# Optimization experiments

Hardware: AMD Instinct MI355X
Metric: run time of the kernel (lower is better)

## Reference

```python
import jax, jax.numpy as jnp
import numpy as np

D_MODEL = 256
N_HEAD = 8
D_FF = 2048
BATCH = 4
TOK_PER_BATCH = 4096
N = BATCH * TOK_PER_BATCH  # 16384 total queries == total keys
L = 32  # neighbors per query
EPS = 1e-5


def _layer_norm(x, g, b):
    mu = jnp.mean(x, axis=-1, keepdims=True)
    var = jnp.mean(jnp.square(x - mu), axis=-1, keepdims=True)
    return (x - mu) * jax.lax.rsqrt(var + EPS) * g + b


def setup_inputs() -> dict:
    key = jax.random.key(0)
    ks = jax.random.split(key, 16)
    d, f = D_MODEL, D_FF
    s = 1.0 / np.sqrt(d)
    inp = {
        "src": jax.random.normal(ks[0], (N, d), dtype=jnp.float32),
        "index_pair": jax.random.randint(ks[1], (N, L), 0, TOK_PER_BATCH, dtype=jnp.int64),
        "query_batch_cnt": jnp.full((BATCH,), TOK_PER_BATCH, dtype=jnp.int32),
        "key_batch_cnt": jnp.full((BATCH,), TOK_PER_BATCH, dtype=jnp.int32),
        "index_pair_batch": jnp.repeat(jnp.arange(BATCH, dtype=jnp.int32), TOK_PER_BATCH),
        "Wq": jax.random.normal(ks[2], (d, d), dtype=jnp.float32) * s,
        "bq": jnp.zeros((d,), jnp.float32),
        "Wk": jax.random.normal(ks[3], (d, d), dtype=jnp.float32) * s,
        "bk": jnp.zeros((d,), jnp.float32),
        "Wv": jax.random.normal(ks[4], (d, d), dtype=jnp.float32) * s,
        "bv": jnp.zeros((d,), jnp.float32),
        "Wo": jax.random.normal(ks[5], (d, d), dtype=jnp.float32) * s,
        "bo": jnp.zeros((d,), jnp.float32),
        "W1": jax.random.normal(ks[6], (d, f), dtype=jnp.float32) * s,
        "b1": jnp.zeros((f,), jnp.float32),
        "W2": jax.random.normal(ks[7], (f, d), dtype=jnp.float32) * (1.0 / np.sqrt(f)),
        "b2": jnp.zeros((d,), jnp.float32),
        "g1": jnp.ones((d,), jnp.float32),
        "be1": jnp.zeros((d,), jnp.float32),
        "g2": jnp.ones((d,), jnp.float32),
        "be2": jnp.zeros((d,), jnp.float32),
    }
    return inp


def _attention(src, index_pair, key_batch_cnt, index_pair_batch,
               Wq, bq, Wk, bk, Wv, bv, Wo, bo):
    n, d = src.shape
    hd = d // N_HEAD
    scale = hd ** -0.5
    q = (src @ Wq + bq).reshape(n, N_HEAD, hd) * scale
    k = src @ Wk + bk
    v = src @ Wv + bv
    # exclusive cumsum -> start offset of each batch's key segment
    key_start = jnp.cumsum(key_batch_cnt) - key_batch_cnt          # [B]
    offs = key_start[index_pair_batch]                             # [N]
    valid = index_pair >= 0                                        # [N, L]
    idx = jnp.where(valid, index_pair + offs[:, None].astype(index_pair.dtype), 0)
    kg = k[idx].reshape(n, L, N_HEAD, hd)                          # gathered keys
    vg = v[idx].reshape(n, L, N_HEAD, hd)                          # gathered values
    logits = jnp.einsum("nhd,nlhd->nhl", q, kg)
    logits = jnp.where(valid[:, None, :], logits, jnp.float32(-1e9))
    attn = jax.nn.softmax(logits, axis=-1)
    out = jnp.einsum("nhl,nlhd->nhd", attn, vg).reshape(n, d)
    return out @ Wo + bo


def reference(src, index_pair, query_batch_cnt, key_batch_cnt, index_pair_batch,
              Wq, bq, Wk, bk, Wv, bv, Wo, bo, W1, b1, W2, b2, g1, be1, g2, be2):
    src2 = _attention(src, index_pair, key_batch_cnt, index_pair_batch,
                      Wq, bq, Wk, bk, Wv, bv, Wo, bo)
    x = _layer_norm(src + src2, g1, be1)
    ff = jax.nn.relu(x @ W1 + b1) @ W2 + b2
    return _layer_norm(x + ff, g2, be2)
```

## Files before the change

### kernel.cpp

```cpp
#include <hip/hip_runtime.h>
#include <hip/hip_bf16.h>
#include <cstddef>
#include <cstdint>

#define D_MODEL 256
#define N_TOK   16384
#define NHEAD   8
#define HDIM    32
#define LNEIGH  32
#define DFF     2048

typedef short bf16x8 __attribute__((ext_vector_type(8)));
typedef float f32x4  __attribute__((ext_vector_type(4)));

__device__ __forceinline__ float b2f(short s) {
    unsigned u = ((unsigned)(unsigned short)s) << 16;
    return __builtin_bit_cast(float, u);
}

__device__ __forceinline__ void gload_lds16(const void* g, void* l) {
    auto* gp = reinterpret_cast<const __attribute__((address_space(1))) uint32_t*>(
        reinterpret_cast<uintptr_t>(g));
    auto* lp = reinterpret_cast<__attribute__((address_space(3))) uint32_t*>(
        reinterpret_cast<uintptr_t>(l));
    __builtin_amdgcn_global_load_lds(gp, lp, 16, 0, 0);
}

__global__ __launch_bounds__(256) void gemm_bt(
    const __hip_bfloat16* __restrict__ A, int lda,
    const __hip_bfloat16* __restrict__ Bt, int ldb,
    const float* __restrict__ bias,
    __hip_bfloat16* __restrict__ outb,
    int M, int N, int K, int relu)
{
    __shared__ short Asm[2][128 * 32];
    __shared__ short Bsm[2][128 * 32];

    const int tid  = threadIdx.x;
    const int lane = tid & 63;
    const int wid  = tid >> 6;
    const int wr   = wid >> 1;
    const int wc   = wid & 1;
    const int bm   = blockIdx.y * 128;
    const int bn   = blockIdx.x * 128;

    f32x4 acc[4][4] = {};
    const int srow = lane >> 2;
    const int seg  = (lane & 3) * 8;

    auto stage = [&](int buf, int k0) {
        #pragma unroll
        for (int t = 0; t < 2; ++t) {
            int rbase = wid * 32 + t * 16;
            gload_lds16(A  + (size_t)(bm + rbase + srow) * lda + k0 + seg, &Asm[buf][rbase * 32]);
            gload_lds16(Bt + (size_t)(bn + rbase + srow) * ldb + k0 + seg, &Bsm[buf][rbase * 32]);
        }
    };

    const int nk = K >> 5;
    stage(0, 0);
    __syncthreads();

    for (int kk = 0; kk < nk; ++kk) {
        const int cur = kk & 1;
        if (kk + 1 < nk) stage(cur ^ 1, (kk + 1) << 5);

        bf16x8 a[4], b[4];
        #pragma unroll
        for (int i = 0; i < 4; ++i)
            a[i] = *(const bf16x8*)&Asm[cur][(wr * 64 + i * 16 + (lane & 15)) * 32 + (lane >> 4) * 8];
        #pragma unroll
        for (int j = 0; j < 4; ++j)
            b[j] = *(const bf16x8*)&Bsm[cur][(wc * 64 + j * 16 + (lane & 15)) * 32 + (lane >> 4) * 8];
        #pragma unroll
        for (int i = 0; i < 4; ++i)
            #pragma unroll
            for (int j = 0; j < 4; ++j)
                acc[i][j] = __builtin_amdgcn_mfma_f32_16x16x32_bf16(a[i], b[j], acc[i][j], 0, 0, 0);
        __syncthreads();
    }

    #pragma unroll
    for (int i = 0; i < 4; ++i) {
        int rbase = bm + wr * 64 + i * 16 + ((lane >> 4) << 2);
        #pragma unroll
        for (int j = 0; j < 4; ++j) {
            int col = bn + wc * 64 + j * 16 + (lane & 15);
            float bval = bias ? bias[col] : 0.0f;
            #pragma unroll
            for (int r = 0; r < 4; ++r) {
                int row = rbase + r;
                float v = acc[i][j][r] + bval;
                if (relu) v = fmaxf(v, 0.0f);
                outb[(size_t)row * N + col] = __float2bfloat16(v);
            }
        }
    }
}

__global__ __launch_bounds__(256) void gemm_qkv(
    const __hip_bfloat16* __restrict__ A,
    const __hip_bfloat16* __restrict__ Bt,
    const float* __restrict__ bias,
    float* __restrict__ qf,
    __hip_bfloat16* __restrict__ kvb)
{
    __shared__ short Asm[2][128 * 32];
    __shared__ short Bsm[2][128 * 32];

    const int tid  = threadIdx.x;
    const int lane = tid & 63;
    const int wid  = tid >> 6;
    const int wr   = wid >> 1;
    const int wc   = wid & 1;
    const int bm   = blockIdx.y * 128;
    const int bn   = blockIdx.x * 128;

    f32x4 acc[4][4] = {};
    const int srow = lane >> 2;
    const int seg  = (lane & 3) * 8;

    auto stage = [&](int buf, int k0) {
        #pragma unroll
        for (int t = 0; t < 2; ++t) {
            int rbase = wid * 32 + t * 16;
            gload_lds16(A  + (size_t)(bm + rbase + srow) * 256 + k0 + seg, &Asm[buf][rbase * 32]);
            gload_lds16(Bt + (size_t)(bn + rbase + srow) * 256 + k0 + seg, &Bsm[buf][rbase * 32]);
        }
    };

    stage(0, 0);
    __syncthreads();
    for (int kk = 0; kk < 8; ++kk) {
        const int cur = kk & 1;
        if (kk + 1 < 8) stage(cur ^ 1, (kk + 1) << 5);
        bf16x8 a[4], b[4];
        #pragma unroll
        for (int i = 0; i < 4; ++i)
            a[i] = *(const bf16x8*)&Asm[cur][(wr * 64 + i * 16 + (lane & 15)) * 32 + (lane >> 4) * 8];
        #pragma unroll
        for (int j = 0; j < 4; ++j)
            b[j] = *(const bf16x8*)&Bsm[cur][(wc * 64 + j * 16 + (lane & 15)) * 32 + (lane >> 4) * 8];
        #pragma unroll
        for (int i = 0; i < 4; ++i)
            #pragma unroll
            for (int j = 0; j < 4; ++j)
                acc[i][j] = __builtin_amdgcn_mfma_f32_16x16x32_bf16(a[i], b[j], acc[i][j], 0, 0, 0);
        __syncthreads();
    }

    const bool isq = (bn < 256);
    #pragma unroll
    for (int i = 0; i < 4; ++i) {
        int rbase = bm + wr * 64 + i * 16 + ((lane >> 4) << 2);
        #pragma unroll
        for (int j = 0; j < 4; ++j) {
            int col = bn + wc * 64 + j * 16 + (lane & 15);
            float bval = bias[col];
            #pragma unroll
            for (int r = 0; r < 4; ++r) {
                int row = rbase + r;
                float v = acc[i][j][r] + bval;
                if (isq) qf[(size_t)row * 256 + col] = v;
                else     kvb[(size_t)row * 512 + (col - 256)] = __float2bfloat16(v);
            }
        }
    }
}

__global__ __launch_bounds__(512) void gemm_bt_ln8(
    const __hip_bfloat16* __restrict__ A, int lda,
    const __hip_bfloat16* __restrict__ Bt, int ldb,
    const float* __restrict__ bias,
    const float* __restrict__ residf,
    const __hip_bfloat16* __restrict__ residb,
    const float* __restrict__ g,
    const float* __restrict__ be,
    float* __restrict__ outf,
    __hip_bfloat16* __restrict__ outb,
    int K)
{
    __shared__ short Asm[2][64 * 32];
    __shared__ short Bsm[2][256 * 32];
    __shared__ float lnS[8][64], lnS2[8][64];
    __shared__ float rmu[64], rrs[64];

    const int tid  = threadIdx.x;
    const int lane = tid & 63;
    const int wid  = tid >> 6;
    const int wr   = wid >> 2;
    const int wc   = wid & 3;
    const int bm   = blockIdx.x * 64;
    const int lo   = lane & 15;
    const int hi   = lane >> 4;

    f32x4 acc[2][4] = {};
    const int srow = lane >> 2;
    const int seg  = (lane & 3) * 8;

    auto stage = [&](int buf, int k0) {
        if (wid < 4) {
            int ra = wid * 16;
            gload_lds16(A + (size_t)(bm + ra + srow) * lda + k0 + seg, &Asm[buf][ra * 32]);
        }
        #pragma unroll
        for (int t = 0; t < 2; ++t) {
            int rb = wid * 32 + t * 16;
            gload_lds16(Bt + (size_t)(rb + srow) * ldb + k0 + seg, &Bsm[buf][rb * 32]);
        }
    };

    const int nk = K >> 5;
    stage(0, 0);
    __syncthreads();

    for (int kk = 0; kk < nk; ++kk) {
        const int cur = kk & 1;
        if (kk + 1 < nk) stage(cur ^ 1, (kk + 1) << 5);

        bf16x8 a[2], b[4];
        #pragma unroll
        for (int i = 0; i < 2; ++i)
            a[i] = *(const bf16x8*)&Asm[cur][(wr * 32 + i * 16 + lo) * 32 + hi * 8];
        #pragma unroll
        for (int j = 0; j < 4; ++j)
            b[j] = *(const bf16x8*)&Bsm[cur][(wc * 64 + j * 16 + lo) * 32 + hi * 8];
        #pragma unroll
        for (int i = 0; i < 2; ++i)
            #pragma unroll
            for (int j = 0; j < 4; ++j)
                acc[i][j] = __builtin_amdgcn_mfma_f32_16x16x32_bf16(a[i], b[j], acc[i][j], 0, 0, 0);
        __syncthreads();
    }

    float ps[2][4] = {}, ps2[2][4] = {};
    #pragma unroll
    for (int j = 0; j < 4; ++j) {
        int col = wc * 64 + j * 16 + lo;
        float bval = bias ? bias[col] : 0.0f;
        #pragma unroll
        for (int i = 0; i < 2; ++i) {
            #pragma unroll
            for (int r = 0; r < 4; ++r) {
                int row = bm + wr * 32 + i * 16 + hi * 4 + r;
                float v = acc[i][j][r] + bval;
                size_t o = (size_t)row * 256 + col;
                if (residf) v += residf[o];
                if (residb) v += __bfloat162float(residb[o]);
                acc[i][j][r] = v;
                ps[i][r]  += v;
                ps2[i][r] += v * v;
            }
        }
    }
    #pragma unroll
    for (int i = 0; i < 2; ++i)
        #pragma unroll
        for (int r = 0; r < 4; ++r) {
            #pragma unroll
            for (int m = 1; m < 16; m <<= 1) {
                ps[i][r]  += __shfl_xor(ps[i][r],  m);
                ps2[i][r] += __shfl_xor(ps2[i][r], m);
            }
        }
    if (lo == 0) {
        #pragma unroll
        for (int i = 0; i < 2; ++i)
            #pragma unroll
            for (int r = 0; r < 4; ++r) {
                int rl = wr * 32 + i * 16 + hi * 4 + r;
                lnS[wid][rl]  = ps[i][r];
                lnS2[wid][rl] = ps2[i][r];
            }
    }
    __syncthreads();
    if (tid < 64) {
        int base = (tid >> 5) * 4;
        float s  = lnS[base][tid] + lnS[base + 1][tid] + lnS[base + 2][tid] + lnS[base + 3][tid];
        float s2 = lnS2[base][tid] + lnS2[base + 1][tid] + lnS2[base + 2][tid] + lnS2[base + 3][tid];
        float mu  = s * (1.0f / 256.0f);
        float var = s2 * (1.0f / 256.0f) - mu * mu;
        rmu[tid] = mu;
        rrs[tid] = rsqrtf(var + 1e-5f);
    }
    __syncthreads();

    #pragma unroll
    for (int j = 0; j < 4; ++j) {
        int col = wc * 64 + j * 16 + lo;
        float gg = g[col], bb = be[col];
        #pragma unroll
        for (int i = 0; i < 2; ++i) {
            #pragma unroll
            for (int r = 0; r < 4; ++r) {
                int rl = wr * 32 + i * 16 + hi * 4 + r;
                float v = (acc[i][j][r] - rmu[rl]) * rrs[rl] * gg + bb;
                size_t o = (size_t)(bm + rl) * 256 + col;
                if (outf) outf[o] = v;
                if (outb) outb[o] = __float2bfloat16(v);
            }
        }
    }
}

__global__ __launch_bounds__(256) void cvt_f2b(
    const float* __restrict__ x, __hip_bfloat16* __restrict__ y, int n)
{
    int i = (blockIdx.x * 256 + threadIdx.x) * 4;
    if (i >= n) return;
    float4 v = *(const float4*)(x + i);
    y[i + 0] = __float2bfloat16(v.x);
    y[i + 1] = __float2bfloat16(v.y);
    y[i + 2] = __float2bfloat16(v.z);
    y[i + 3] = __float2bfloat16(v.w);
}

__global__ __launch_bounds__(256) void cvt_wt_tiled(
    const float* __restrict__ W, __hip_bfloat16* __restrict__ Wt,
    int K, int N, float scale)
{
    __shared__ float t[32][33];
    const int n0 = blockIdx.x * 32;
    const int k0 = blockIdx.y * 32;
    const int tx = threadIdx.x & 31;
    const int ty = threadIdx.x >> 5;
    #pragma unroll
    for (int i = 0; i < 32; i += 8)
        t[ty + i][tx] = W[(size_t)(k0 + ty + i) * N + n0 + tx];
    __syncthreads();
    #pragma unroll
    for (int i = 0; i < 32; i += 8)
        Wt[(size_t)(n0 + ty + i) * K + k0 + tx] = __float2bfloat16(t[tx][ty + i] * scale);
}

__global__ __launch_bounds__(256) void cvt_w3_tiled(
    const float* __restrict__ Wa, const float* __restrict__ Wb,
    const float* __restrict__ Wc, __hip_bfloat16* __restrict__ Wt,
    float scale_a)
{
    __shared__ float t[32][33];
    const int n0 = blockIdx.x * 32;
    const int k0 = blockIdx.y * 32;
    const float* W = (n0 < 256) ? Wa : (n0 < 512 ? Wb : Wc);
    const float sc = (n0 < 256) ? scale_a : 1.0f;
    const int ncol = n0 & 255;
    const int tx = threadIdx.x & 31;
    const int ty = threadIdx.x >> 5;
    #pragma unroll
    for (int i = 0; i < 32; i += 8)
        t[ty + i][tx] = W[(size_t)(k0 + ty + i) * 256 + ncol + tx];
    __syncthreads();
    #pragma unroll
    for (int i = 0; i < 32; i += 8)
        Wt[(size_t)(n0 + ty + i) * 256 + k0 + tx] = __float2bfloat16(t[tx][ty + i] * sc);
}

__global__ __launch_bounds__(768) void make_bqkv(
    const float* __restrict__ bq, const float* __restrict__ bk,
    const float* __restrict__ bv, const int* __restrict__ kbc, int nb,
    float* __restrict__ o, int* __restrict__ ks, float qs)
{
    int i = threadIdx.x;
    if (i < 256)      o[i] = bq[i] * qs;
    else if (i < 512) o[i] = bk[i - 256];
    else              o[i] = bv[i - 512];
    if (i < nb) {
        int acc = 0;
        for (int j = 0; j < i; ++j) acc += kbc[j];
        ks[i] = acc;
    }
}

__global__ __launch_bounds__(256) void attn_wave(
    const float* __restrict__ qf,
    const __hip_bfloat16* __restrict__ kvb,
    const int* __restrict__ index_pair,
    const int* __restrict__ ipb,
    const int* __restrict__ key_start,
    __hip_bfloat16* __restrict__ out)
{
    const int w    = threadIdx.x >> 6;
    const int lane = threadIdx.x & 63;
    const int bid  = blockIdx.x;
    const int n  = (bid & 7) * 2048 + (bid >> 3) * 4 + w;
    const int c  = lane & 31;
    const int pp = lane >> 5;

    int raw = index_pair[(size_t)n * LNEIGH + c];
    int ks  = key_start[ipb[n]];
    int gi0 = (raw >= 0) ? raw + ks : -1;

    const float* qp = qf + (size_t)n * 256 + c * 8;
    float4 q0 = *(const float4*)(qp);
    float4 q1 = *(const float4*)(qp + 4);

    int gi[16];
    #pragma unroll
    for (int i = 0; i < 16; ++i) gi[i] = __shfl(gi0, 2 * i + pp);

    bf16x8 kr[16];
    #pragma unroll
    for (int i = 0; i < 16; ++i) {
        int g = gi[i] < 0 ? 0 : gi[i];
        kr[i] = *(const bf16x8*)(kvb + (size_t)g * 512 + c * 8);
    }

    float s[16];
    #pragma unroll
    for (int i = 0; i < 16; ++i) {
        float t = q0.x * b2f(kr[i][0]) + q0.y * b2f(kr[i][1])
                + q0.z * b2f(kr[i][2]) + q0.w * b2f(kr[i][3])
                + q1.x * b2f(kr[i][4]) + q1.y * b2f(kr[i][5])
                + q1.z * b2f(kr[i][6]) + q1.w * b2f(kr[i][7]);
        t += __shfl_xor(t, 1);
        t += __shfl_xor(t, 2);
        s[i] = (gi[i] < 0) ? -1e9f : t;
    }

    bf16x8 vr[16];
    #pragma unroll
    for (int i = 0; i < 16; ++i) {
        int g = gi[i] < 0 ? 0 : gi[i];
        vr[i] = *(const bf16x8*)(kvb + (size_t)g * 512 + 256 + c * 8);
    }

    float m = s[0];
    #pragma unroll
    for (int i = 1; i < 16; ++i) m = fmaxf(m, s[i]);
    m = fmaxf(m, __shfl_xor(m, 32));
    float tot = 0.0f;
    #pragma unroll
    for (int i = 0; i < 16; ++i) { s[i] = __expf(s[i] - m); tot += s[i]; }
    tot += __shfl_xor(tot, 32);
    const float inv = 1.0f / tot;

    float a[8] = {};
    #pragma unroll
    for (int i = 0; i < 16; ++i) {
        float wt = s[i] * inv;
        #pragma unroll
        for (int j = 0; j < 8; ++j) a[j] += wt * b2f(vr[i][j]);
    }
    #pragma unroll
    for (int j = 0; j < 8; ++j) a[j] += __shfl_xor(a[j], 32);

    if (pp == 0) {
        bf16x8 ov;
        #pragma unroll
        for (int j = 0; j < 8; ++j)
            ov[j] = __builtin_bit_cast(short, __float2bfloat16(a[j]));
        *(bf16x8*)((short*)out + (size_t)n * 256 + c * 8) = ov;
    }
}

extern "C" void kernel_launch(void* const* d_in, const int* in_sizes, int n_in,
                              void* d_out, int out_size, void* d_ws, size_t ws_size,
                              hipStream_t stream)
{
    const float* src = (const float*)d_in[0];
    const int*   index_pair = (const int*)d_in[1];
    const int*   kbc = (const int*)d_in[3];
    const int*   ipb = (const int*)d_in[4];
    const float* Wq = (const float*)d_in[5];
    const float* bq = (const float*)d_in[6];
    const float* Wk = (const float*)d_in[7];
    const float* bk = (const float*)d_in[8];
    const float* Wv = (const float*)d_in[9];
    const float* bv = (const float*)d_in[10];
    const float* Wo = (const float*)d_in[11];
    const float* bo = (const float*)d_in[12];
    const float* W1 = (const float*)d_in[13];
    const float* b1 = (const float*)d_in[14];
    const float* W2 = (const float*)d_in[15];
    const float* b2 = (const float*)d_in[16];
    const float* g1 = (const float*)d_in[17];
    const float* be1 = (const float*)d_in[18];
    const float* g2 = (const float*)d_in[19];
    const float* be2 = (const float*)d_in[20];
    float* out = (float*)d_out;
    const int nb = in_sizes[3];

    char* ws = (char*)d_ws;
    const size_t O_SRCBF = 0;
    const size_t O_QF    = 8388608;
    const size_t O_KVB   = 25165824;
    const size_t O_ATTN  = 41943040;
    const size_t O_HC    = 0;
    const size_t O_XBF   = 67108864;
    const size_t O_WQKV  = 75497472;
    const size_t O_WO    = O_WQKV + 768 * 256 * 2;
    const size_t O_W1    = O_WO + 256 * 256 * 2;
    const size_t O_W2    = O_W1 + (size_t)DFF * 256 * 2;
    const size_t O_BQKV  = O_W2 + (size_t)DFF * 256 * 2;
    const size_t O_KS    = O_BQKV + 768 * 4;

    __hip_bfloat16* src_bf  = (__hip_bfloat16*)(ws + O_SRCBF);
    float*          qf      = (float*)(ws + O_QF);
    __hip_bfloat16* kvb     = (__hip_bfloat16*)(ws + O_KVB);
    __hip_bfloat16* attn_bf = (__hip_bfloat16*)(ws + O_ATTN);
    __hip_bfloat16* hc      = (__hip_bfloat16*)(ws + O_HC);
    __hip_bfloat16* x_bf    = (__hip_bfloat16*)(ws + O_XBF);
    __hip_bfloat16* WqkvT   = (__hip_bfloat16*)(ws + O_WQKV);
    __hip_bfloat16* WoT     = (__hip_bfloat16*)(ws + O_WO);
    __hip_bfloat16* W1T     = (__hip_bfloat16*)(ws + O_W1);
    __hip_bfloat16* W2T     = (__hip_bfloat16*)(ws + O_W2);
    float*          bqkv    = (float*)(ws + O_BQKV);
    int*            ksbuf   = (int*)(ws + O_KS);

    const dim3 blk(256);
    const float qscale = 0.17677669529663687f;

    cvt_f2b<<<N_TOK * D_MODEL / 4 / 256, blk, 0, stream>>>(src, src_bf, N_TOK * D_MODEL);
    cvt_w3_tiled<<<dim3(24, 8), blk, 0, stream>>>(Wq, Wk, Wv, WqkvT, qscale);
    cvt_wt_tiled<<<dim3(8, 8),  blk, 0, stream>>>(Wo, WoT, 256, 256, 1.0f);
    cvt_wt_tiled<<<dim3(64, 8), blk, 0, stream>>>(W1, W1T, 256, DFF, 1.0f);
    cvt_wt_tiled<<<dim3(8, 64), blk, 0, stream>>>(W2, W2T, DFF, 256, 1.0f);
    make_bqkv<<<1, 768, 0, stream>>>(bq, bk, bv, kbc, nb, bqkv, ksbuf, qscale);

    gemm_qkv<<<dim3(6, 128), blk, 0, stream>>>(src_bf, WqkvT, bqkv, qf, kvb);

    attn_wave<<<dim3(N_TOK / 4), blk, 0, stream>>>(qf, kvb, index_pair, ipb, ksbuf, attn_bf);

    gemm_bt_ln8<<<dim3(N_TOK / 64), dim3(512), 0, stream>>>(
        attn_bf, 256, WoT, 256, bo, src, nullptr, g1, be1,
        nullptr, x_bf, 256);

    gemm_bt<<<dim3(16, 128), blk, 0, stream>>>(
        x_bf, 256, W1T, 256, b1, hc, N_TOK, DFF, 256, 1);

    gemm_bt_ln8<<<dim3(N_TOK / 64), dim3(512), 0, stream>>>(
        hc, DFF, W2T, DFF, b2, nullptr, x_bf, g2, be2,
        out, nullptr, DFF);
}
```

Before: 169.4 us.

## Load GEMM+LayerNorm operands straight from global memory and pad hidden leading dimension

The fused GEMM+LayerNorm kernel no longer stages A and B tiles through shared memory. Each wave now loads its MFMA fragments directly from global memory, which removes the LDS traffic and the per-step barriers. The FFN hidden activation and transposed W2 get a padded leading dimension (2080 instead of 2048) to break power-of-two strides that would otherwise cause channel or cache conflicts on the direct loads. The cost is that B fragments are reread from global/L2 by every wave with no shared reuse, and the loads are strided gathers rather than coalesced tiles.

Measured after the change: 202.8 us. +19.7%, slower.

```diff
diff --git a/kernel.cpp b/kernel.cpp
--- a/kernel.cpp
+++ b/kernel.cpp
@@ -9,6 +9,7 @@
 #define HDIM    32
 #define LNEIGH  32
 #define DFF     2048
+#define HCP     2080
 
 typedef short bf16x8 __attribute__((ext_vector_type(8)));
 typedef float f32x4  __attribute__((ext_vector_type(4)));
@@ -30,7 +31,7 @@
     const __hip_bfloat16* __restrict__ A, int lda,
     const __hip_bfloat16* __restrict__ Bt, int ldb,
     const float* __restrict__ bias,
-    __hip_bfloat16* __restrict__ outb,
+    __hip_bfloat16* __restrict__ outb, int ldc,
     int M, int N, int K, int relu)
 {
     __shared__ short Asm[2][128 * 32];
@@ -92,83 +93,13 @@
                 int row = rbase + r;
                 float v = acc[i][j][r] + bval;
                 if (relu) v = fmaxf(v, 0.0f);
-                outb[(size_t)row * N + col] = __float2bfloat16(v);
+                outb[(size_t)row * ldc + col] = __float2bfloat16(v);
             }
         }
     }
 }
 
-__global__ __launch_bounds__(256) void gemm_qkv(
-    const __hip_bfloat16* __restrict__ A,
-    const __hip_bfloat16* __restrict__ Bt,
-    const float* __restrict__ bias,
-    float* __restrict__ qf,
-    __hip_bfloat16* __restrict__ kvb)
-{
-    __shared__ short Asm[2][128 * 32];
-    __shared__ short Bsm[2][128 * 32];
-
-    const int tid  = threadIdx.x;
-    const int lane = tid & 63;
-    const int wid  = tid >> 6;
-    const int wr   = wid >> 1;
-    const int wc   = wid & 1;
-    const int bm   = blockIdx.y * 128;
-    const int bn   = blockIdx.x * 128;
-
-    f32x4 acc[4][4] = {};
-    const int srow = lane >> 2;
-    const int seg  = (lane & 3) * 8;
-
-    auto stage = [&](int buf, int k0) {
-        #pragma unroll
-        for (int t = 0; t < 2; ++t) {
-            int rbase = wid * 32 + t * 16;
-            gload_lds16(A  + (size_t)(bm + rbase + srow) * 256 + k0 + seg, &Asm[buf][rbase * 32]);
-            gload_lds16(Bt + (size_t)(bn + rbase + srow) * 256 + k0 + seg, &Bsm[buf][rbase * 32]);
-        }
-    };
-
-    stage(0, 0);
-    __syncthreads();
-    for (int kk = 0; kk < 8; ++kk) {
-        const int cur = kk & 1;
-        if (kk + 1 < 8) stage(cur ^ 1, (kk + 1) << 5);
-        bf16x8 a[4], b[4];
-        #pragma unroll
-        for (int i = 0; i < 4; ++i)
-            a[i] = *(const bf16x8*)&Asm[cur][(wr * 64 + i * 16 + (lane & 15)) * 32 + (lane >> 4) * 8];
-        #pragma unroll
-        for (int j = 0; j < 4; ++j)
-            b[j] = *(const bf16x8*)&Bsm[cur][(wc * 64 + j * 16 + (lane & 15)) * 32 + (lane >> 4) * 8];
-        #pragma unroll
-        for (int i = 0; i < 4; ++i)
-            #pragma unroll
-            for (int j = 0; j < 4; ++j)
-                acc[i][j] = __builtin_amdgcn_mfma_f32_16x16x32_bf16(a[i], b[j], acc[i][j], 0, 0, 0);
-        __syncthreads();
-    }
-
-    const bool isq = (bn < 256);
-    #pragma unroll
-    for (int i = 0; i < 4; ++i) {
-        int rbase = bm + wr * 64 + i * 16 + ((lane >> 4) << 2);
-        #pragma unroll
-        for (int j = 0; j < 4; ++j) {
-            int col = bn + wc * 64 + j * 16 + (lane & 15);
-            float bval = bias[col];
-            #pragma unroll
-            for (int r = 0; r < 4; ++r) {
-                int row = rbase + r;
-                float v = acc[i][j][r] + bval;
-                if (isq) qf[(size_t)row * 256 + col] = v;
-                else     kvb[(size_t)row * 512 + (col - 256)] = __float2bfloat16(v);
-            }
-        }
-    }
-}
-
-__global__ __launch_bounds__(512) void gemm_bt_ln8(
+__global__ __launch_bounds__(512) void gemm_nolds_ln(
     const __hip_bfloat16* __restrict__ A, int lda,
     const __hip_bfloat16* __restrict__ Bt, int ldb,
     const float* __restrict__ bias,
@@ -180,8 +111,6 @@
     __hip_bfloat16* __restrict__ outb,
     int K)
 {
-    __shared__ short Asm[2][64 * 32];
-    __shared__ short Bsm[2][256 * 32];
     __shared__ float lnS[8][64], lnS2[8][64];
     __shared__ float rmu[64], rrs[64];
 
@@ -195,42 +124,32 @@
     const int hi   = lane >> 4;
 
     f32x4 acc[2][4] = {};
-    const int srow = lane >> 2;
-    const int seg  = (lane & 3) * 8;
-
-    auto stage = [&](int buf, int k0) {
-        if (wid < 4) {
-            int ra = wid * 16;
-            gload_lds16(A + (size_t)(bm + ra + srow) * lda + k0 + seg, &Asm[buf][ra * 32]);
-        }
-        #pragma unroll
-        for (int t = 0; t < 2; ++t) {
-            int rb = wid * 32 + t * 16;
-            gload_lds16(Bt + (size_t)(rb + srow) * ldb + k0 + seg, &Bsm[buf][rb * 32]);
-        }
-    };
+
+    const __hip_bfloat16* arow0 = A + (size_t)(bm + wr * 32 + lo) * lda + hi * 8;
+    const __hip_bfloat16* arow1 = arow0 + (size_t)16 * lda;
+    const __hip_bfloat16* brow[4];
+    #pragma unroll
+    for (int j = 0; j < 4; ++j)
+        brow[j] = Bt + (size_t)(wc * 64 + j * 16 + lo) * ldb + hi * 8;
 
     const int nk = K >> 5;
-    stage(0, 0);
-    __syncthreads();
-
+    #pragma unroll 2
     for (int kk = 0; kk < nk; ++kk) {
-        const int cur = kk & 1;
-        if (kk + 1 < nk) stage(cur ^ 1, (kk + 1) << 5);
-
-        bf16x8 a[2], b[4];
-        #pragma unroll
-        for (int i = 0; i < 2; ++i)
-            a[i] = *(const bf16x8*)&Asm[cur][(wr * 32 + i * 16 + lo) * 32 + hi * 8];
-        #pragma unroll
-        for (int j = 0; j < 4; ++j)
-            b[j] = *(const bf16x8*)&Bsm[cur][(wc * 64 + j * 16 + lo) * 32 + hi * 8];
-        #pragma unroll
-        for (int i = 0; i < 2; ++i)
-            #pragma unroll
-            for (int j = 0; j < 4; ++j)
-                acc[i][j] = __builtin_amdgcn_mfma_f32_16x16x32_bf16(a[i], b[j], acc[i][j], 0, 0, 0);
-        __syncthreads();
+        const int ko = kk * 32;
+        bf16x8 a0 = *(const bf16x8*)(arow0 + ko);
+        bf16x8 a1 = *(const bf16x8*)(arow1 + ko);
+        bf16x8 b0 = *(const bf16x8*)(brow[0] + ko);
+        bf16x8 b1 = *(const bf16x8*)(brow[1] + ko);
+        bf16x8 b2 = *(const bf16x8*)(brow[2] + ko);
+        bf16x8 b3 = *(const bf16x8*)(brow[3] + ko);
+        acc[0][0] = __builtin_amdgcn_mfma_f32_16x16x32_bf16(a0, b0, acc[0][0], 0, 0, 0);
+        acc[0][1] = __builtin_amdgcn_mfma_f32_16x16x32_bf16(a0, b1, acc[0][1], 0, 0, 0);
+        acc[0][2] = __builtin_amdgcn_mfma_f32_16x16x32_bf16(a0, b2, acc[0][2], 0, 0, 0);
+        acc[0][3] = __builtin_amdgcn_mfma_f32_16x16x32_bf16(a0, b3, acc[0][3], 0, 0, 0);
+        acc[1][0] = __builtin_amdgcn_mfma_f32_16x16x32_bf16(a1, b0, acc[1][0], 0, 0, 0);
+        acc[1][1] = __builtin_amdgcn_mfma_f32_16x16x32_bf16(a1, b1, acc[1][1], 0, 0, 0);
+        acc[1][2] = __builtin_amdgcn_mfma_f32_16x16x32_bf16(a1, b2, acc[1][2], 0, 0, 0);
+        acc[1][3] = __builtin_amdgcn_mfma_f32_16x16x32_bf16(a1, b3, acc[1][3], 0, 0, 0);
     }
 
     float ps[2][4] = {}, ps2[2][4] = {};
@@ -303,6 +222,76 @@
     }
 }
 
+__global__ __launch_bounds__(256) void gemm_qkv(
+    const __hip_bfloat16* __restrict__ A,
+    const __hip_bfloat16* __restrict__ Bt,
+    const float* __restrict__ bias,
+    float* __restrict__ qf,
+    __hip_bfloat16* __restrict__ kvb)
+{
+    __shared__ short Asm[2][128 * 32];
+    __shared__ short Bsm[2][128 * 32];
+
+    const int tid  = threadIdx.x;
+    const int lane = tid & 63;
+    const int wid  = tid >> 6;
+    const int wr   = wid >> 1;
+    const int wc   = wid & 1;
+    const int bm   = blockIdx.y * 128;
+    const int bn   = blockIdx.x * 128;
+
+    f32x4 acc[4][4] = {};
+    const int srow = lane >> 2;
+    const int seg  = (lane & 3) * 8;
+
+    auto stage = [&](int buf, int k0) {
+        #pragma unroll
+        for (int t = 0; t < 2; ++t) {
+            int rbase = wid * 32 + t * 16;
+            gload_lds16(A  + (size_t)(bm + rbase + srow) * 256 + k0 + seg, &Asm[buf][rbase * 32]);
+            gload_lds16(Bt + (size_t)(bn + rbase + srow) * 256 + k0 + seg, &Bsm[buf][rbase * 32]);
+        }
+    };
+
+    stage(0, 0);
+    __syncthreads();
+    for (int kk = 0; kk < 8; ++kk) {
+        const int cur = kk & 1;
+        if (kk + 1 < 8) stage(cur ^ 1, (kk + 1) << 5);
+        bf16x8 a[4], b[4];
+        #pragma unroll
+        for (int i = 0; i < 4; ++i)
+            a[i] = *(const bf16x8*)&Asm[cur][(wr * 64 + i * 16 + (lane & 15)) * 32 + (lane >> 4) * 8];
+        #pragma unroll
+        for (int j = 0; j < 4; ++j)
+            b[j] = *(const bf16x8*)&Bsm[cur][(wc * 64 + j * 16 + (lane & 15)) * 32 + (lane >> 4) * 8];
+        #pragma unroll
+        for (int i = 0; i < 4; ++i)
+            #pragma unroll
+            for (int j = 0; j < 4; ++j)
+                acc[i][j] = __builtin_amdgcn_mfma_f32_16x16x32_bf16(a[i], b[j], acc[i][j], 0, 0, 0);
+        __syncthreads();
+    }
+
+    const bool isq = (bn < 256);
+    #pragma unroll
+    for (int i = 0; i < 4; ++i) {
+        int rbase = bm + wr * 64 + i * 16 + ((lane >> 4) << 2);
+        #pragma unroll
+        for (int j = 0; j < 4; ++j) {
+            int col = bn + wc * 64 + j * 16 + (lane & 15);
+            float bval = bias[col];
+            #pragma unroll
+            for (int r = 0; r < 4; ++r) {
+                int row = rbase + r;
+                float v = acc[i][j][r] + bval;
+                if (isq) qf[(size_t)row * 256 + col] = v;
+                else     kvb[(size_t)row * 512 + (col - 256)] = __float2bfloat16(v);
+            }
+        }
+    }
+}
+
 __global__ __launch_bounds__(256) void cvt_f2b(
     const float* __restrict__ x, __hip_bfloat16* __restrict__ y, int n)
 {
@@ -317,7 +306,7 @@
 
 __global__ __launch_bounds__(256) void cvt_wt_tiled(
     const float* __restrict__ W, __hip_bfloat16* __restrict__ Wt,
-    int K, int N, float scale)
+    int K, int N, int ldo, float scale)
 {
     __shared__ float t[32][33];
     const int n0 = blockIdx.x * 32;
@@ -330,7 +319,7 @@
     __syncthreads();
     #pragma unroll
     for (int i = 0; i < 32; i += 8)
-        Wt[(size_t)(n0 + ty + i) * K + k0 + tx] = __float2bfloat16(t[tx][ty + i] * scale);
+        Wt[(size_t)(n0 + ty + i) * ldo + k0 + tx] = __float2bfloat16(t[tx][ty + i] * scale);
 }
 
 __global__ __launch_bounds__(256) void cvt_w3_tiled(
@@ -481,18 +470,18 @@
     const int nb = in_sizes[3];
 
     char* ws = (char*)d_ws;
+    const size_t O_HC    = 0;
     const size_t O_SRCBF = 0;
     const size_t O_QF    = 8388608;
     const size_t O_KVB   = 25165824;
     const size_t O_ATTN  = 41943040;
-    const size_t O_HC    = 0;
-    const size_t O_XBF   = 67108864;
-    const size_t O_WQKV  = 75497472;
+    const size_t O_XBF   = 68157440;
+    const size_t O_WQKV  = 76546048;
     const size_t O_WO    = O_WQKV + 768 * 256 * 2;
     const size_t O_W1    = O_WO + 256 * 256 * 2;
     const size_t O_W2    = O_W1 + (size_t)DFF * 256 * 2;
-    const size_t O_BQKV  = O_W2 + (size_t)DFF * 256 * 2;
-    const size_t O_KS    = O_BQKV + 768 * 4;
+    const size_t O_BQKV  = O_W2 + (size_t)256 * HCP * 2;
+    const size_t O_KS    = O_BQKV + 4096;
 
     __hip_bfloat16* src_bf  = (__hip_bfloat16*)(ws + O_SRCBF);
     float*          qf      = (float*)(ws + O_QF);
@@ -512,23 +501,23 @@
 
     cvt_f2b<<<N_TOK * D_MODEL / 4 / 256, blk, 0, stream>>>(src, src_bf, N_TOK * D_MODEL);
     cvt_w3_tiled<<<dim3(24, 8), blk, 0, stream>>>(Wq, Wk, Wv, WqkvT, qscale);
-    cvt_wt_tiled<<<dim3(8, 8),  blk, 0, stream>>>(Wo, WoT, 256, 256, 1.0f);
-    cvt_wt_tiled<<<dim3(64, 8), blk, 0, stream>>>(W1, W1T, 256, DFF, 1.0f);
-    cvt_wt_tiled<<<dim3(8, 64), blk, 0, stream>>>(W2, W2T, DFF, 256, 1.0f);
+    cvt_wt_tiled<<<dim3(8, 8),  blk, 0, stream>>>(Wo, WoT, 256, 256, 256, 1.0f);
+    cvt_wt_tiled<<<dim3(64, 8), blk, 0, stream>>>(W1, W1T, 256, DFF, 256, 1.0f);
+    cvt_wt_tiled<<<dim3(8, 64), blk, 0, stream>>>(W2, W2T, DFF, 256, HCP, 1.0f);
     make_bqkv<<<1, 768, 0, stream>>>(bq, bk, bv, kbc, nb, bqkv, ksbuf, qscale);
 
     gemm_qkv<<<dim3(6, 128), blk, 0, stream>>>(src_bf, WqkvT, bqkv, qf, kvb);
 
     attn_wave<<<dim3(N_TOK / 4), blk, 0, stream>>>(qf, kvb, index_pair, ipb, ksbuf, attn_bf);
 
-    gemm_bt_ln8<<<dim3(N_TOK / 64), dim3(512), 0, stream>>>(
+    gemm_nolds_ln<<<dim3(N_TOK / 64), dim3(512), 0, stream>>>(
         attn_bf, 256, WoT, 256, bo, src, nullptr, g1, be1,
         nullptr, x_bf, 256);
 
     gemm_bt<<<dim3(16, 128), blk, 0, stream>>>(
-        x_bf, 256, W1T, 256, b1, hc, N_TOK, DFF, 256, 1);
-
-    gemm_bt_ln8<<<dim3(N_TOK / 64), dim3(512), 0, stream>>>(
-        hc, DFF, W2T, DFF, b2, nullptr, x_bf, g2, be2,
+        x_bf, 256, W1T, 256, b1, hc, HCP, N_TOK, DFF, 256, 1);
+
+    gemm_nolds_ln<<<dim3(N_TOK / 64), dim3(512), 0, stream>>>(
+        hc, HCP, W2T, HCP, b2, nullptr, x_bf, g2, be2,
         out, nullptr, DFF);
 }
```
